# Kernel optimization log

Measured on AMD Instinct MI355X. Metric: run time of the kernel, lower is better.

## Reference

```python
import jax, jax.numpy as jnp
import numpy as np

N, E, G, D = 100000, 1600000, 1000, 32
EPS = 1e-5


def setup_inputs() -> dict:
    key = jax.random.key(0)
    ks = jax.random.split(key, 24)
    inp = {
        'h': jax.random.normal(ks[0], (N, D), dtype=jnp.float32),
        'src': jax.random.randint(ks[1], (E,), 0, N, dtype=jnp.int32),
        'dst': jax.random.randint(ks[2], (E,), 0, N, dtype=jnp.int32),
        'graph_id': jnp.sort(jax.random.randint(ks[3], (N,), 0, G, dtype=jnp.int32)),
    }
    dims = [D, 32, 32, 32, 1]
    ki = 4
    for i in range(4):
        inp[f'conv_w{i}'] = jax.random.normal(ks[ki], (dims[i], dims[i + 1]), dtype=jnp.float32) * 0.1; ki += 1
        inp[f'conv_b{i}'] = jax.random.normal(ks[ki], (dims[i + 1],), dtype=jnp.float32) * 0.1; ki += 1
        inp[f'bn_g{i}'] = jnp.ones((dims[i + 1],), dtype=jnp.float32)
        inp[f'bn_b{i}'] = jnp.zeros((dims[i + 1],), dtype=jnp.float32)
    mlp_dims = [D + 32 + 32 + 32 + 1, 128, 64, 1]  # 129 -> 128 -> 64 -> 1
    for i in range(3):
        inp[f'mlp_w{i}'] = jax.random.normal(ks[ki], (mlp_dims[i], mlp_dims[i + 1]), dtype=jnp.float32) * 0.1; ki += 1
        inp[f'mlp_b{i}'] = jax.random.normal(ks[ki], (mlp_dims[i + 1],), dtype=jnp.float32) * 0.1; ki += 1
    return inp


def _mean_agg(x, src, dst):
    # DGL update_all(copy_u, mean): h'_v = mean of h_u over in-neighbors u of v
    deg = jax.ops.segment_sum(jnp.ones((src.shape[0],), x.dtype), dst, num_segments=N)
    agg = jax.ops.segment_sum(x[src], dst, num_segments=N)
    return agg / jnp.maximum(deg, 1.0)[:, None]


def _bn(x, g, b):
    # BatchNorm1d in training mode: batch statistics over node dim
    m = x.mean(axis=0)
    v = x.var(axis=0)
    return g * (x - m) * jax.lax.rsqrt(v + EPS) + b


def reference(h, src, dst, graph_id,
              conv_w0, conv_b0, conv_w1, conv_b1, conv_w2, conv_b2, conv_w3, conv_b3,
              bn_g0, bn_b0, bn_g1, bn_b1, bn_g2, bn_b2, bn_g3, bn_b3,
              mlp_w0, mlp_b0, mlp_w1, mlp_b1, mlp_w2, mlp_b2):
    conv = [(conv_w0, conv_b0), (conv_w1, conv_b1), (conv_w2, conv_b2), (conv_w3, conv_b3)]
    bn = [(bn_g0, bn_b0), (bn_g1, bn_b1), (bn_g2, bn_b2), (bn_g3, bn_b3)]
    h_list = [h]
    x = h
    for (w, b), (g, bb) in zip(conv, bn):
        x = _mean_agg(x, src, dst) @ w + b      # GCNConv
        x = jax.nn.relu(_bn(x, g, bb))           # BN + ReLU
        h_list.append(x)
    h_final = jnp.concatenate(h_list, axis=1)    # [N, 129]
    # dgl.mean_nodes: per-graph mean pool
    cnt = jax.ops.segment_sum(jnp.ones((N,), h_final.dtype), graph_id, num_segments=G)
    hg = jax.ops.segment_sum(h_final, graph_id, num_segments=G) / jnp.maximum(cnt, 1.0)[:, None]
    hg = jax.nn.relu(hg @ mlp_w0 + mlp_b0)
    hg = jax.nn.relu(hg @ mlp_w1 + mlp_b1)
    hg = hg @ mlp_w2 + mlp_b2
    return hg.reshape(-1)                         # [G]
```

## Files before the change

### kernel.cpp

```cpp
#include <hip/hip_runtime.h>

#define NSLOT 32
#define BN_EPS 1e-5f
#define NSB 256
#define BKBITS 8
#define BKN 256
#define MAXBUCK 512

static inline int cdiv_h(int a, int b) { return (a + b - 1) / b; }

__device__ __forceinline__ float4 f4add(float4 a, float4 b) {
    return make_float4(a.x + b.x, a.y + b.y, a.z + b.z, a.w + b.w);
}

__device__ __forceinline__ unsigned bf16rtn(float x) {
    unsigned u = __float_as_uint(x);
    return (u + 0x7FFFu + ((u >> 16) & 1u)) >> 16;
}
__device__ __forceinline__ unsigned bf16pack2(float lo, float hi) {
    return bf16rtn(lo) | (bf16rtn(hi) << 16);
}

__device__ __forceinline__ int blk_excl_scan256(int v, int t) {
    __shared__ int wsum[4];
    int l = t & 63, w = t >> 6;
    int incl = v;
#pragma unroll
    for (int off = 1; off < 64; off <<= 1) {
        int o = __shfl_up(incl, off, 64);
        if (l >= off) incl += o;
    }
    if (l == 63) wsum[w] = incl;
    __syncthreads();
    int wofs = 0;
#pragma unroll
    for (int i = 0; i < 4; i++) wofs += (i < w) ? wsum[i] : 0;
    __syncthreads();
    return wofs + incl - v;
}

__device__ __forceinline__ int blk_excl_scan512(int v, int t) {
    __shared__ int wsum8[8];
    int l = t & 63, w = t >> 6;
    int incl = v;
#pragma unroll
    for (int off = 1; off < 64; off <<= 1) {
        int o = __shfl_up(incl, off, 64);
        if (l >= off) incl += o;
    }
    if (l == 63) wsum8[w] = incl;
    __syncthreads();
    int wofs = 0;
#pragma unroll
    for (int i = 0; i < 8; i++) wofs += (i < w) ? wsum8[i] : 0;
    __syncthreads();
    return wofs + incl - v;
}


__global__ __launch_bounds__(256) void k_hist(const int* __restrict__ dst, int* __restrict__ histT,
                                              int E, int nbuck, int chunk) {
    __shared__ int bins[MAXBUCK];
    int k = blockIdx.x, t = threadIdx.x;
    for (int b = t; b < nbuck; b += 256) bins[b] = 0;
    __syncthreads();
    int lo = k * chunk, hi = lo + chunk; if (hi > E) hi = E;
    for (int i = lo + t; i < hi; i += 256) atomicAdd(&bins[dst[i] >> BKBITS], 1);
    __syncthreads();
    for (int b = t; b < nbuck; b += 256) histT[k * nbuck + b] = bins[b];
}


__global__ __launch_bounds__(256) void k_scanA(const int* __restrict__ histT, int* __restrict__ prefixB,
                                               int* __restrict__ totalP, int* __restrict__ totalU, int nbuck) {
    int b = blockIdx.x, k = threadIdx.x;
    int c = histT[k * nbuck + b];
    int pad = (c + 15) & ~15;
    int ep = blk_excl_scan256(pad, k);
    prefixB[b * NSB + k] = ep;
    int ec = blk_excl_scan256(c, k);
    if (k == NSB - 1) { totalP[b] = ep + pad; totalU[b] = ec + c; }
}

__global__ __launch_bounds__(512) void k_scanB(const int* __restrict__ totalP, const int* __restrict__ totalU,
                                               int* __restrict__ baseP, int* __restrict__ baseU, int nbuck) {
    int t = threadIdx.x;
    int vp = (t < nbuck) ? totalP[t] : 0;
    int vu = (t < nbuck) ? totalU[t] : 0;
    int ep = blk_excl_scan512(vp, t);
    int eu = blk_excl_scan512(vu, t);
    if (t < nbuck) { baseP[t] = ep; baseU[t] = eu; }
}


__global__ __launch_bounds__(256) void k_scatter2(const int* __restrict__ src, const int* __restrict__ dst,
                                                  const int* __restrict__ baseP, const int* __restrict__ prefixB,
                                                  unsigned* __restrict__ ebuf, int E, int nbuck, int chunk) {
    __shared__ int cur[MAXBUCK];
    int k = blockIdx.x, t = threadIdx.x;
    for (int b = t; b < nbuck; b += 256) cur[b] = baseP[b] + prefixB[b * NSB + k];
    __syncthreads();
    int lo = k * chunk, hi = lo + chunk; if (hi > E) hi = E;
    for (int i = lo + t; i < hi; i += 256) {
        int d = dst[i], s = src[i];
        int b = d >> BKBITS;
        int pos = atomicAdd(&cur[b], 1);
        ebuf[pos] = ((unsigned)(d & (BKN - 1)) << 24) | (unsigned)s;
    }
}


__global__ __launch_bounds__(256) void k_sortb(const unsigned* __restrict__ ebuf, const int* __restrict__ histT,
                                               const int* __restrict__ baseP, const int* __restrict__ prefixB,
                                               const int* __restrict__ baseU,
                                               int* __restrict__ col, int* __restrict__ rs, int* __restrict__ re,
                                               int nbuck, int N) {
    __shared__ int binCnt[BKN], binStart[BKN], cursor[BKN];
    __shared__ int cellBase[NSB], cellCnt[NSB];
    int b = blockIdx.x, t = threadIdx.x;
    cellBase[t] = baseP[b] + prefixB[b * NSB + t];
    cellCnt[t]  = histT[t * nbuck + b];
    binCnt[t] = 0; cursor[t] = 0;
    __syncthreads();
    {
        int cb = cellBase[t], cc = cellCnt[t];
        for (int j = 0; j < cc; j++) atomicAdd(&binCnt[ebuf[cb + j] >> 24], 1);
    }
    __syncthreads();
    int bs = blk_excl_scan256(binCnt[t], t);
    binStart[t] = bs;
    __syncthreads();
    int colBase = baseU[b];
    {
        int cb = cellBase[t], cc = cellCnt[t];
        for (int j = 0; j < cc; j++) {
            unsigned e = ebuf[cb + j];
            int l = e >> 24;
            int pos = binStart[l] + atomicAdd(&cursor[l], 1);
            col[colBase + pos] = (int)(e & 0xFFFFFFu);
        }
    }
    int node = b * BKN + t;
    if (node < N) {
        rs[node] = colBase + binStart[t];
        re[node] = colBase + binStart[t] + binCnt[t];
    }
}


__global__ __launch_bounds__(256) void k_gstart(const int* __restrict__ gid, int* __restrict__ gstart, int n, int G) {
    int i = blockIdx.x * 256 + threadIdx.x;
    if (i >= n) return;
    int g = gid[i];
    int gp = (i == 0) ? -1 : gid[i - 1];
    for (int x = gp + 1; x <= g; ++x) gstart[x] = i;
    if (i == n - 1) { for (int x = g + 1; x <= G; ++x) gstart[x] = n; }
}


template <int AFF>
__global__ __launch_bounds__(256) void k_transform(const float* __restrict__ xin, const float* __restrict__ W,
                                                   const float* __restrict__ cA, const float* __restrict__ cC,
                                                   uint4* __restrict__ pb, int n) {
    __shared__ float sW[32][32];
    __shared__ float sA[32], sC[32];
    int t = threadIdx.x;
    for (int i = t; i < 1024; i += 256) sW[i >> 5][i & 31] = W[i];
    if (AFF && t < 32) { sA[t] = cA[t]; sC[t] = cC[t]; }
    __syncthreads();
    int node = blockIdx.x * 256 + t;
    if (node >= n) return;
    float x[32];
    const float4* s4 = (const float4*)(xin + (size_t)node * 32);
#pragma unroll
    for (int q = 0; q < 8; q++) {
        float4 v = s4[q];
        x[4*q] = v.x; x[4*q+1] = v.y; x[4*q+2] = v.z; x[4*q+3] = v.w;
    }
    if (AFF) {
#pragma unroll
        for (int k = 0; k < 32; k++) {
            float v = sA[k] * x[k] + sC[k];
            x[k] = v > 0.f ? v : 0.f;
        }
    }
    float acc[32];
#pragma unroll
    for (int f = 0; f < 32; f++) acc[f] = 0.f;
#pragma unroll
    for (int k = 0; k < 32; k++) {
        float xv = x[k];
#pragma unroll
        for (int f = 0; f < 32; f++) acc[f] += xv * sW[k][f];
    }
    uint4* d4 = pb + (size_t)node * 4;
#pragma unroll
    for (int q = 0; q < 4; q++) {
        uint4 o;
        o.x = bf16pack2(acc[8*q+0], acc[8*q+1]);
        o.y = bf16pack2(acc[8*q+2], acc[8*q+3]);
        o.z = bf16pack2(acc[8*q+4], acc[8*q+5]);
        o.w = bf16pack2(acc[8*q+6], acc[8*q+7]);
        d4[q] = o;
    }
}

__global__ __launch_bounds__(256) void k_transform3(const float* __restrict__ y2, const float* __restrict__ w3,
                                                    const float* __restrict__ cA, const float* __restrict__ cC,
                                                    float* __restrict__ p3, int n) {
    __shared__ float sw[32], sA[32], sC[32];
    int t = threadIdx.x;
    if (t < 32) { sw[t] = w3[t]; sA[t] = cA[t]; sC[t] = cC[t]; }
    __syncthreads();
    int i = blockIdx.x * 256 + t;
    if (i >= n) return;
    const float4* x4 = (const float4*)(y2 + (size_t)i * 32);
    float acc = 0.f;
#pragma unroll
    for (int q = 0; q < 8; q++) {
        float4 v = x4[q];
        float vv[4] = {v.x, v.y, v.z, v.w};
#pragma unroll
        for (int r = 0; r < 4; r++) {
            int k = q * 4 + r;
            float xv = sA[k] * vv[r] + sC[k];
            xv = xv > 0.f ? xv : 0.f;
            acc += xv * sw[k];
        }
    }
    p3[i] = acc;
}


__global__ __launch_bounds__(256) void k_aggregate(const uint4* __restrict__ pb, const int* __restrict__ rs,
                                                   const int* __restrict__ re, const int* __restrict__ col,
                                                   const float* __restrict__ bias,
                                                   float4* __restrict__ y4, float* __restrict__ sSum,
                                                   float* __restrict__ sSq, int n) {
    int t = threadIdx.x;
    int lane = t & 3;
    int grp = t >> 2;
    int node = blockIdx.x * 64 + grp;
    float accA[8], accB[8];
#pragma unroll
    for (int q = 0; q < 8; q++) { accA[q] = 0.f; accB[q] = 0.f; }
    float vout[8];
#pragma unroll
    for (int q = 0; q < 8; q++) vout[q] = 0.f;
    if (node < n) {
        int s0 = rs[node], s1 = re[node];
        int j = s0;
#define GATH(vv, c) uint4 vv = pb[(size_t)(c) * 4 + lane]
#define ACC(dst, vv) \
        dst[0] += __uint_as_float((vv).x << 16); dst[1] += __uint_as_float((vv).x & 0xFFFF0000u); \
        dst[2] += __uint_as_float((vv).y << 16); dst[3] += __uint_as_float((vv).y & 0xFFFF0000u); \
        dst[4] += __uint_as_float((vv).z << 16); dst[5] += __uint_as_float((vv).z & 0xFFFF0000u); \
        dst[6] += __uint_as_float((vv).w << 16); dst[7] += __uint_as_float((vv).w & 0xFFFF0000u)
        for (; j + 8 <= s1; j += 8) {
            int c0 = col[j], c1 = col[j + 1], c2 = col[j + 2], c3 = col[j + 3];
            int c4 = col[j + 4], c5 = col[j + 5], c6 = col[j + 6], c7 = col[j + 7];
            GATH(g0, c0); GATH(g1, c1); GATH(g2, c2); GATH(g3, c3);
            GATH(g4, c4); GATH(g5, c5); GATH(g6, c6); GATH(g7, c7);
            ACC(accA, g0); ACC(accB, g1); ACC(accA, g2); ACC(accB, g3);
            ACC(accA, g4); ACC(accB, g5); ACC(accA, g6); ACC(accB, g7);
        }
        for (; j < s1; ++j) {
            GATH(g, col[j]);
            ACC(accA, g);
        }
#undef GATH
#undef ACC
        int deg = s1 - s0;
        float inv = (deg > 0) ? 1.f / (float)deg : 1.f;
        const float4* b4 = (const float4*)bias;
        float4 b0 = b4[lane * 2], b1 = b4[lane * 2 + 1];
        vout[0] = (accA[0] + accB[0]) * inv + b0.x;
        vout[1] = (accA[1] + accB[1]) * inv + b0.y;
        vout[2] = (accA[2] + accB[2]) * inv + b0.z;
        vout[3] = (accA[3] + accB[3]) * inv + b0.w;
        vout[4] = (accA[4] + accB[4]) * inv + b1.x;
        vout[5] = (accA[5] + accB[5]) * inv + b1.y;
        vout[6] = (accA[6] + accB[6]) * inv + b1.z;
        vout[7] = (accA[7] + accB[7]) * inv + b1.w;
        y4[(size_t)node * 8 + lane * 2]     = make_float4(vout[0], vout[1], vout[2], vout[3]);
        y4[(size_t)node * 8 + lane * 2 + 1] = make_float4(vout[4], vout[5], vout[6], vout[7]);
    }
    __shared__ float sS[64][32];
    __shared__ float sQ[64][32];
    ((float4*)&sS[grp][lane * 8])[0] = make_float4(vout[0], vout[1], vout[2], vout[3]);
    ((float4*)&sS[grp][lane * 8])[1] = make_float4(vout[4], vout[5], vout[6], vout[7]);
    ((float4*)&sQ[grp][lane * 8])[0] = make_float4(vout[0]*vout[0], vout[1]*vout[1], vout[2]*vout[2], vout[3]*vout[3]);
    ((float4*)&sQ[grp][lane * 8])[1] = make_float4(vout[4]*vout[4], vout[5]*vout[5], vout[6]*vout[6], vout[7]*vout[7]);
    __syncthreads();
    if (t < 32) {
        float S = 0.f, Q = 0.f;
#pragma unroll
        for (int g2 = 0; g2 < 64; g2++) { S += sS[g2][t]; Q += sQ[g2][t]; }
        int slot = blockIdx.x & (NSLOT - 1);
        atomicAdd(&sSum[slot * 32 + t], S);
        atomicAdd(&sSq[slot * 32 + t], Q);
    }
}

__global__ __launch_bounds__(256) void k_aggregate3(const float* __restrict__ p3, const int* __restrict__ rs,
                                                    const int* __restrict__ re, const int* __restrict__ col,
                                                    const float* __restrict__ b1,
                                                    float* __restrict__ y3, float* __restrict__ sSum,
                                                    float* __restrict__ sSq, int n) {
    int i = blockIdx.x * 256 + threadIdx.x;
    float lsum = 0.f, lsq = 0.f;
    if (i < n) {
        int s0 = rs[i], s1 = re[i];
        float a0 = 0.f, a1 = 0.f, a2 = 0.f, a3 = 0.f;
        int j = s0;
        for (; j + 4 <= s1; j += 4) {
            int c0 = col[j], c1 = col[j + 1], c2 = col[j + 2], c3 = col[j + 3];
            a0 += p3[c0]; a1 += p3[c1]; a2 += p3[c2]; a3 += p3[c3];
        }
        for (; j < s1; ++j) a0 += p3[col[j]];
        float acc = (a0 + a1) + (a2 + a3);
        float inv = (s1 > s0) ? 1.f / (float)(s1 - s0) : 1.f;
        float v = acc * inv + b1[0];
        y3[i] = v; lsum = v; lsq = v * v;
    }
    __shared__ float sS[256], sQ[256];
    int t = threadIdx.x;
    sS[t] = lsum; sQ[t] = lsq;
    __syncthreads();
    for (int s = 128; s > 0; s >>= 1) {
        if (t < s) { sS[t] += sS[t + s]; sQ[t] += sQ[t + s]; }
        __syncthreads();
    }
    if (t == 0) {
        int slot = blockIdx.x & (NSLOT - 1);
        atomicAdd(&sSum[slot * 32], sS[0]);
        atomicAdd(&sSq[slot * 32], sQ[0]);
    }
}


__global__ void k_stats(const float* __restrict__ sSum, const float* __restrict__ sSq,
                        const float* __restrict__ g, const float* __restrict__ b,
                        float* __restrict__ cA, float* __restrict__ cC, int C, float invN) {
    int f = threadIdx.x;
    if (f < C) {
        float S = 0.f, Q = 0.f;
        for (int s = 0; s < NSLOT; s++) { S += sSum[s * 32 + f]; Q += sSq[s * 32 + f]; }
        float m = S * invN;
        float var = Q * invN - m * m;
        if (var < 0.f) var = 0.f;
        float inv = rsqrtf(var + BN_EPS);
        float a = g[f] * inv;
        cA[f] = a;
        cC[f] = b[f] - m * a;
    }
}


__global__ __launch_bounds__(256) void k_pool_mlp(const float* __restrict__ h, const float* __restrict__ y0,
                                                  const float* __restrict__ y1, const float* __restrict__ y2,
                                                  const float* __restrict__ y3, const float* __restrict__ cA,
                                                  const float* __restrict__ cC, const int* __restrict__ gstart,
                                                  const float* __restrict__ w0, const float* __restrict__ b0,
                                                  const float* __restrict__ w1, const float* __restrict__ b1,
                                                  const float* __restrict__ w2, const float* __restrict__ b2,
                                                  float* __restrict__ out) {
    int g = blockIdx.x;
    int t = threadIdx.x;
    int s0 = gstart[g], s1 = gstart[g + 1];
    int lane = t & 31, slot = t >> 5;
    int arr = lane >> 3, sub = lane & 7;
    const float* bases0 = (arr == 0) ? h : (arr == 1) ? y0 : (arr == 2) ? y1 : y2;
    const float4* bp = (const float4*)bases0;
    float4 a4 = make_float4(1.f, 1.f, 1.f, 1.f);
    float4 c4 = make_float4(0.f, 0.f, 0.f, 0.f);
    bool aff = (arr > 0);
    if (aff) {
        a4 = ((const float4*)cA)[(arr - 1) * 8 + sub];
        c4 = ((const float4*)cC)[(arr - 1) * 8 + sub];
    }
    float4 acc = make_float4(0.f, 0.f, 0.f, 0.f);
    for (int n = s0 + slot; n < s1; n += 8) {
        float4 v = bp[(size_t)n * 8 + sub];
        if (aff) {
            float vx = fmaf(a4.x, v.x, c4.x); vx = vx > 0.f ? vx : 0.f;
            float vy = fmaf(a4.y, v.y, c4.y); vy = vy > 0.f ? vy : 0.f;
            float vz = fmaf(a4.z, v.z, c4.z); vz = vz > 0.f ? vz : 0.f;
            float vw = fmaf(a4.w, v.w, c4.w); vw = vw > 0.f ? vw : 0.f;
            v = make_float4(vx, vy, vz, vw);
        }
        acc = f4add(acc, v);
    }
    __shared__ float sP[8][128];
    __shared__ float sY[8];
    ((float4*)&sP[slot][lane * 4])[0] = acc;
    if (t < 8) {
        float a = cA[96], c = cC[96], s = 0.f;
        for (int n = s0 + t; n < s1; n += 8) {
            float v = fmaf(a, y3[n], c);
            s += v > 0.f ? v : 0.f;
        }
        sY[t] = s;
    }
    __syncthreads();
    __shared__ float hg[129];
    __shared__ float hid1[128];
    __shared__ float hid2[64];
    float inv = (s1 > s0) ? 1.f / (float)(s1 - s0) : 1.f;
    if (t < 128) {
        float S = 0.f;
#pragma unroll
        for (int s = 0; s < 8; s++) S += sP[s][t];
        hg[t] = S * inv;
    } else if (t == 128) {
        float S = 0.f;
#pragma unroll
        for (int s = 0; s < 8; s++) S += sY[s];
        hg[128] = S * inv;
    }
    __syncthreads();
    if (t < 128) {
        float a = b0[t];
        for (int i = 0; i < 129; i++) a += hg[i] * w0[i * 128 + t];
        hid1[t] = a > 0.f ? a : 0.f;
    }
    __syncthreads();
    if (t < 64) {
        float a = b1[t];
        for (int i = 0; i < 128; i++) a += hid1[i] * w1[i * 64 + t];
        hid2[t] = a > 0.f ? a : 0.f;
    }
    __syncthreads();
    if (t < 64) {
        float v = hid2[t] * w2[t];
        for (int off = 32; off > 0; off >>= 1) v += __shfl_down(v, off, 64);
        if (t == 0) out[g] = v + b2[0];
    }
}


extern "C" void kernel_launch(void* const* d_in, const int* in_sizes, int n_in,
                              void* d_out, int out_size, void* d_ws, size_t ws_size,
                              hipStream_t stream) {
    const float* h   = (const float*)d_in[0];
    const int* src   = (const int*)d_in[1];
    const int* dst   = (const int*)d_in[2];
    const int* gid   = (const int*)d_in[3];
    const float* convw[4], *convb[4], *bng[4], *bnb[4];
    for (int i = 0; i < 4; i++) {
        convw[i] = (const float*)d_in[4 + 4 * i];
        convb[i] = (const float*)d_in[5 + 4 * i];
        bng[i]   = (const float*)d_in[6 + 4 * i];
        bnb[i]   = (const float*)d_in[7 + 4 * i];
    }
    const float* mw0 = (const float*)d_in[20];
    const float* mb0 = (const float*)d_in[21];
    const float* mw1 = (const float*)d_in[22];
    const float* mb1 = (const float*)d_in[23];
    const float* mw2 = (const float*)d_in[24];
    const float* mb2 = (const float*)d_in[25];

    const int N = in_sizes[0] / 32;
    const int E = in_sizes[1];
    const int G = out_size;
    const int nbuck = cdiv_h(N, BKN);
    const int chunk = cdiv_h(E, NSB);

    char* ws = (char*)d_ws;
    size_t off = 0;
    auto alloc = [&](size_t bytes) -> void* {
        void* p = ws + off;
        off += (bytes + 511) & ~(size_t)511;
        return p;
    };
    int* histT   = (int*)alloc((size_t)NSB * nbuck * 4);
    int* prefixB = (int*)alloc((size_t)nbuck * NSB * 4);
    int* totalP  = (int*)alloc((size_t)nbuck * 4);
    int* totalU  = (int*)alloc((size_t)nbuck * 4);
    int* basePp  = (int*)alloc((size_t)nbuck * 4);
    int* baseUp  = (int*)alloc((size_t)nbuck * 4);
    size_t ebufE = (size_t)E + (size_t)16 * NSB * nbuck;
    size_t ovl   = ebufE * 4;
    size_t pB    = (size_t)N * 64;
    if (pB > ovl) ovl = pB;
    unsigned* ebuf = (unsigned*)alloc(ovl);
    uint4* pb    = (uint4*)ebuf;
    int* col     = (int*)alloc((size_t)E * 4);
    int* rs      = (int*)alloc((size_t)N * 4);
    int* re      = (int*)alloc((size_t)N * 4);
    int* gstart  = (int*)alloc((size_t)(G + 1) * 4);
    float* y0    = (float*)alloc((size_t)N * 32 * 4);
    float* y1    = (float*)alloc((size_t)N * 32 * 4);
    float* y2    = (float*)alloc((size_t)N * 32 * 4);
    float* y3    = (float*)alloc((size_t)N * 4);
    float* sSum  = (float*)alloc((size_t)4 * NSLOT * 32 * 4);
    float* sSq   = (float*)alloc((size_t)4 * NSLOT * 32 * 4);
    float* cAa   = (float*)alloc((size_t)4 * 32 * 4);
    float* cCc   = (float*)alloc((size_t)4 * 32 * 4);
    (void)ws_size; (void)n_in;

    const int NB_N = cdiv_h(N, 256);
    const int NB_AG = cdiv_h(N, 64);
    const float invN = 1.f / (float)N;

    hipMemsetAsync(sSum, 0, (size_t)4 * NSLOT * 32 * 4, stream);
    hipMemsetAsync(sSq, 0, (size_t)4 * NSLOT * 32 * 4, stream);

    k_hist<<<NSB, 256, 0, stream>>>(dst, histT, E, nbuck, chunk);
    k_scanA<<<nbuck, 256, 0, stream>>>(histT, prefixB, totalP, totalU, nbuck);
    k_scanB<<<1, 512, 0, stream>>>(totalP, totalU, basePp, baseUp, nbuck);
    k_scatter2<<<NSB, 256, 0, stream>>>(src, dst, basePp, prefixB, ebuf, E, nbuck, chunk);
    k_sortb<<<nbuck, 256, 0, stream>>>(ebuf, histT, basePp, prefixB, baseUp, col, rs, re, nbuck, N);
    k_gstart<<<NB_N, 256, 0, stream>>>(gid, gstart, N, G);

    k_transform<0><<<NB_N, 256, 0, stream>>>(h, convw[0], nullptr, nullptr, pb, N);
    k_aggregate<<<NB_AG, 256, 0, stream>>>(pb, rs, re, col, convb[0], (float4*)y0,
                                           sSum + 0 * NSLOT * 32, sSq + 0 * NSLOT * 32, N);
    k_stats<<<1, 32, 0, stream>>>(sSum + 0 * NSLOT * 32, sSq + 0 * NSLOT * 32, bng[0], bnb[0], cAa + 0, cCc + 0, 32, invN);
    k_transform<1><<<NB_N, 256, 0, stream>>>(y0, convw[1], cAa + 0, cCc + 0, pb, N);
    k_aggregate<<<NB_AG, 256, 0, stream>>>(pb, rs, re, col, convb[1], (float4*)y1,
                                           sSum + 1 * NSLOT * 32, sSq + 1 * NSLOT * 32, N);
    k_stats<<<1, 32, 0, stream>>>(sSum + 1 * NSLOT * 32, sSq + 1 * NSLOT * 32, bng[1], bnb[1], cAa + 32, cCc + 32, 32, invN);
    k_transform<1><<<NB_N, 256, 0, stream>>>(y1, convw[2], cAa + 32, cCc + 32, pb, N);
    k_aggregate<<<NB_AG, 256, 0, stream>>>(pb, rs, re, col, convb[2], (float4*)y2,
                                           sSum + 2 * NSLOT * 32, sSq + 2 * NSLOT * 32, N);
    k_stats<<<1, 32, 0, stream>>>(sSum + 2 * NSLOT * 32, sSq + 2 * NSLOT * 32, bng[2], bnb[2], cAa + 64, cCc + 64, 32, invN);
    k_transform3<<<NB_N, 256, 0, stream>>>(y2, convw[3], cAa + 64, cCc + 64, (float*)pb, N);
    k_aggregate3<<<NB_N, 256, 0, stream>>>((float*)pb, rs, re, col, convb[3], y3,
                                           sSum + 3 * NSLOT * 32, sSq + 3 * NSLOT * 32, N);
    k_stats<<<1, 32, 0, stream>>>(sSum + 3 * NSLOT * 32, sSq + 3 * NSLOT * 32, bng[3], bnb[3], cAa + 96, cCc + 96, 1, invN);

    k_pool_mlp<<<G, 256, 0, stream>>>(h, y0, y1, y2, y3, cAa, cCc, gstart,
                                      mw0, mb0, mw1, mb1, mw2, mb2, (float*)d_out);
}
```

Before: 339.3 us.

## Fold BN stats, memset and gstart into neighbours; stage col indices in LDS

Removes the four single-block BN-statistics kernels by recomputing the BN scale/shift per block inside the consuming transform and pool kernels. It also folds the stats-buffer memsets into k_hist and the graph-start computation into k_scanA, which cuts about seven launches and their serialization gaps. Separately, k_aggregate now cooperatively loads each block's contiguous CSR column range into shared memory before gathering, replacing scattered global index reads. The cost is redundant coefficient recomputation in every block, extra LDS use that may lower occupancy, and removal of the 8-wide unrolled path when the range exceeds 2048 edges.

```diff
diff --git a/kernel.cpp b/kernel.cpp
--- a/kernel.cpp
+++ b/kernel.cpp
@@ -57,11 +57,30 @@
     return wofs + incl - v;
 }
 
+__device__ __forceinline__ void bn_coef(const float* __restrict__ sSum, const float* __restrict__ sSq,
+                                        const float* __restrict__ bg, const float* __restrict__ bb,
+                                        float invN, int ch, float* aOut, float* cOut) {
+    float S = 0.f, Q = 0.f;
+#pragma unroll
+    for (int s = 0; s < NSLOT; s++) { S += sSum[s * 32 + ch]; Q += sSq[s * 32 + ch]; }
+    float m = S * invN;
+    float var = Q * invN - m * m;
+    if (var < 0.f) var = 0.f;
+    float iv = rsqrtf(var + BN_EPS);
+    float a = bg[ch] * iv;
+    *aOut = a;
+    *cOut = bb[ch] - m * a;
+}
+
 
 __global__ __launch_bounds__(256) void k_hist(const int* __restrict__ dst, int* __restrict__ histT,
+                                              float* __restrict__ sSum, float* __restrict__ sSq,
                                               int E, int nbuck, int chunk) {
     __shared__ int bins[MAXBUCK];
     int k = blockIdx.x, t = threadIdx.x;
+    if (k == 0) {
+        for (int i = t; i < 4 * NSLOT * 32; i += 256) { sSum[i] = 0.f; sSq[i] = 0.f; }
+    }
     for (int b = t; b < nbuck; b += 256) bins[b] = 0;
     __syncthreads();
     int lo = k * chunk, hi = lo + chunk; if (hi > E) hi = E;
@@ -72,8 +91,17 @@
 
 
 __global__ __launch_bounds__(256) void k_scanA(const int* __restrict__ histT, int* __restrict__ prefixB,
-                                               int* __restrict__ totalP, int* __restrict__ totalU, int nbuck) {
+                                               int* __restrict__ totalP, int* __restrict__ totalU,
+                                               const int* __restrict__ gid, int* __restrict__ gstart,
+                                               int nbuck, int N, int G) {
     int b = blockIdx.x, k = threadIdx.x;
+    int i = b * 256 + k;
+    if (i < N) {
+        int g = gid[i];
+        int gp = (i == 0) ? -1 : gid[i - 1];
+        for (int x = gp + 1; x <= g; ++x) gstart[x] = i;
+        if (i == N - 1) { for (int x = g + 1; x <= G; ++x) gstart[x] = N; }
+    }
     int c = histT[k * nbuck + b];
     int pad = (c + 15) & ~15;
     int ep = blk_excl_scan256(pad, k);
@@ -148,25 +176,16 @@
 }
 
 
-__global__ __launch_bounds__(256) void k_gstart(const int* __restrict__ gid, int* __restrict__ gstart, int n, int G) {
-    int i = blockIdx.x * 256 + threadIdx.x;
-    if (i >= n) return;
-    int g = gid[i];
-    int gp = (i == 0) ? -1 : gid[i - 1];
-    for (int x = gp + 1; x <= g; ++x) gstart[x] = i;
-    if (i == n - 1) { for (int x = g + 1; x <= G; ++x) gstart[x] = n; }
-}
-
-
 template <int AFF>
 __global__ __launch_bounds__(256) void k_transform(const float* __restrict__ xin, const float* __restrict__ W,
-                                                   const float* __restrict__ cA, const float* __restrict__ cC,
-                                                   uint4* __restrict__ pb, int n) {
+                                                   const float* __restrict__ sSum, const float* __restrict__ sSq,
+                                                   const float* __restrict__ bg, const float* __restrict__ bb,
+                                                   uint4* __restrict__ pb, int n, float invN) {
     __shared__ float sW[32][32];
     __shared__ float sA[32], sC[32];
     int t = threadIdx.x;
     for (int i = t; i < 1024; i += 256) sW[i >> 5][i & 31] = W[i];
-    if (AFF && t < 32) { sA[t] = cA[t]; sC[t] = cC[t]; }
+    if (AFF && t < 32) bn_coef(sSum, sSq, bg, bb, invN, t, &sA[t], &sC[t]);
     __syncthreads();
     int node = blockIdx.x * 256 + t;
     if (node >= n) return;
@@ -206,11 +225,12 @@
 }
 
 __global__ __launch_bounds__(256) void k_transform3(const float* __restrict__ y2, const float* __restrict__ w3,
-                                                    const float* __restrict__ cA, const float* __restrict__ cC,
-                                                    float* __restrict__ p3, int n) {
+                                                    const float* __restrict__ sSum, const float* __restrict__ sSq,
+                                                    const float* __restrict__ bg, const float* __restrict__ bb,
+                                                    float* __restrict__ p3, int n, float invN) {
     __shared__ float sw[32], sA[32], sC[32];
     int t = threadIdx.x;
-    if (t < 32) { sw[t] = w3[t]; sA[t] = cA[t]; sC[t] = cC[t]; }
+    if (t < 32) { sw[t] = w3[t]; bn_coef(sSum, sSq, bg, bb, invN, t, &sA[t], &sC[t]); }
     __syncthreads();
     int i = blockIdx.x * 256 + t;
     if (i >= n) return;
@@ -237,10 +257,22 @@
                                                    const float* __restrict__ bias,
                                                    float4* __restrict__ y4, float* __restrict__ sSum,
                                                    float* __restrict__ sSq, int n) {
+    __shared__ int scol[2048];
     int t = threadIdx.x;
     int lane = t & 3;
     int grp = t >> 2;
-    int node = blockIdx.x * 64 + grp;
+    int node0 = blockIdx.x * 64;
+    int node = node0 + grp;
+    int base0 = 0, len = 0;
+    if (node0 < n) {
+        int last = node0 + 63; if (last > n - 1) last = n - 1;
+        base0 = rs[node0];
+        len = re[last] - base0;
+    }
+    bool lds = (len > 0 && len <= 2048);
+    if (lds) { for (int i = t; i < len; i += 256) scol[i] = col[base0 + i]; }
+    __syncthreads();
+
     float accA[8], accB[8];
 #pragma unroll
     for (int q = 0; q < 8; q++) { accA[q] = 0.f; accB[q] = 0.f; }
@@ -249,24 +281,25 @@
     for (int q = 0; q < 8; q++) vout[q] = 0.f;
     if (node < n) {
         int s0 = rs[node], s1 = re[node];
-        int j = s0;
 #define GATH(vv, c) uint4 vv = pb[(size_t)(c) * 4 + lane]
 #define ACC(dst, vv) \
         dst[0] += __uint_as_float((vv).x << 16); dst[1] += __uint_as_float((vv).x & 0xFFFF0000u); \
         dst[2] += __uint_as_float((vv).y << 16); dst[3] += __uint_as_float((vv).y & 0xFFFF0000u); \
         dst[4] += __uint_as_float((vv).z << 16); dst[5] += __uint_as_float((vv).z & 0xFFFF0000u); \
         dst[6] += __uint_as_float((vv).w << 16); dst[7] += __uint_as_float((vv).w & 0xFFFF0000u)
-        for (; j + 8 <= s1; j += 8) {
-            int c0 = col[j], c1 = col[j + 1], c2 = col[j + 2], c3 = col[j + 3];
-            int c4 = col[j + 4], c5 = col[j + 5], c6 = col[j + 6], c7 = col[j + 7];
-            GATH(g0, c0); GATH(g1, c1); GATH(g2, c2); GATH(g3, c3);
-            GATH(g4, c4); GATH(g5, c5); GATH(g6, c6); GATH(g7, c7);
-            ACC(accA, g0); ACC(accB, g1); ACC(accA, g2); ACC(accB, g3);
-            ACC(accA, g4); ACC(accB, g5); ACC(accA, g6); ACC(accB, g7);
-        }
-        for (; j < s1; ++j) {
-            GATH(g, col[j]);
-            ACC(accA, g);
+        if (lds) {
+            int j = s0 - base0, j1 = s1 - base0;
+            for (; j + 8 <= j1; j += 8) {
+                int c0 = scol[j], c1 = scol[j + 1], c2 = scol[j + 2], c3 = scol[j + 3];
+                int c4 = scol[j + 4], c5 = scol[j + 5], c6 = scol[j + 6], c7 = scol[j + 7];
+                GATH(g0, c0); GATH(g1, c1); GATH(g2, c2); GATH(g3, c3);
+                GATH(g4, c4); GATH(g5, c5); GATH(g6, c6); GATH(g7, c7);
+                ACC(accA, g0); ACC(accB, g1); ACC(accA, g2); ACC(accB, g3);
+                ACC(accA, g4); ACC(accB, g5); ACC(accA, g6); ACC(accB, g7);
+            }
+            for (; j < j1; ++j) { GATH(g, scol[j]); ACC(accA, g); }
+        } else {
+            for (int j = s0; j < s1; ++j) { GATH(g, col[j]); ACC(accA, g); }
         }
 #undef GATH
 #undef ACC
@@ -339,34 +372,30 @@
 }
 
 
-__global__ void k_stats(const float* __restrict__ sSum, const float* __restrict__ sSq,
-                        const float* __restrict__ g, const float* __restrict__ b,
-                        float* __restrict__ cA, float* __restrict__ cC, int C, float invN) {
-    int f = threadIdx.x;
-    if (f < C) {
-        float S = 0.f, Q = 0.f;
-        for (int s = 0; s < NSLOT; s++) { S += sSum[s * 32 + f]; Q += sSq[s * 32 + f]; }
-        float m = S * invN;
-        float var = Q * invN - m * m;
-        if (var < 0.f) var = 0.f;
-        float inv = rsqrtf(var + BN_EPS);
-        float a = g[f] * inv;
-        cA[f] = a;
-        cC[f] = b[f] - m * a;
-    }
-}
-
-
 __global__ __launch_bounds__(256) void k_pool_mlp(const float* __restrict__ h, const float* __restrict__ y0,
                                                   const float* __restrict__ y1, const float* __restrict__ y2,
-                                                  const float* __restrict__ y3, const float* __restrict__ cA,
-                                                  const float* __restrict__ cC, const int* __restrict__ gstart,
+                                                  const float* __restrict__ y3,
+                                                  const float* __restrict__ sSum, const float* __restrict__ sSq,
+                                                  const float* __restrict__ bg0, const float* __restrict__ bb0,
+                                                  const float* __restrict__ bg1, const float* __restrict__ bb1,
+                                                  const float* __restrict__ bg2, const float* __restrict__ bb2,
+                                                  const float* __restrict__ bg3, const float* __restrict__ bb3,
+                                                  const int* __restrict__ gstart,
                                                   const float* __restrict__ w0, const float* __restrict__ b0,
                                                   const float* __restrict__ w1, const float* __restrict__ b1,
                                                   const float* __restrict__ w2, const float* __restrict__ b2,
-                                                  float* __restrict__ out) {
+                                                  float* __restrict__ out, float invN) {
+    __shared__ float pcA[128], pcC[128];
     int g = blockIdx.x;
     int t = threadIdx.x;
+    if (t < 97) {
+        int layer = (t == 96) ? 3 : (t >> 5);
+        int ch = t & 31;
+        const float* bg = (layer == 0) ? bg0 : (layer == 1) ? bg1 : (layer == 2) ? bg2 : bg3;
+        const float* bb = (layer == 0) ? bb0 : (layer == 1) ? bb1 : (layer == 2) ? bb2 : bb3;
+        bn_coef(sSum + layer * NSLOT * 32, sSq + layer * NSLOT * 32, bg, bb, invN, ch, &pcA[t], &pcC[t]);
+    }
+    __syncthreads();
     int s0 = gstart[g], s1 = gstart[g + 1];
     int lane = t & 31, slot = t >> 5;
     int arr = lane >> 3, sub = lane & 7;
@@ -376,8 +405,8 @@
     float4 c4 = make_float4(0.f, 0.f, 0.f, 0.f);
     bool aff = (arr > 0);
     if (aff) {
-        a4 = ((const float4*)cA)[(arr - 1) * 8 + sub];
-        c4 = ((const float4*)cC)[(arr - 1) * 8 + sub];
+        a4 = ((const float4*)pcA)[(arr - 1) * 8 + sub];
+        c4 = ((const float4*)pcC)[(arr - 1) * 8 + sub];
     }
     float4 acc = make_float4(0.f, 0.f, 0.f, 0.f);
     for (int n = s0 + slot; n < s1; n += 8) {
@@ -395,7 +424,7 @@
     __shared__ float sY[8];
     ((float4*)&sP[slot][lane * 4])[0] = acc;
     if (t < 8) {
-        float a = cA[96], c = cC[96], s = 0.f;
+        float a = pcA[96], c = pcC[96], s = 0.f;
         for (int n = s0 + t; n < s1; n += 8) {
             float v = fmaf(a, y3[n], c);
             s += v > 0.f ? v : 0.f;
@@ -495,41 +524,35 @@
     float* y3    = (float*)alloc((size_t)N * 4);
     float* sSum  = (float*)alloc((size_t)4 * NSLOT * 32 * 4);
     float* sSq   = (float*)alloc((size_t)4 * NSLOT * 32 * 4);
-    float* cAa   = (float*)alloc((size_t)4 * 32 * 4);
-    float* cCc   = (float*)alloc((size_t)4 * 32 * 4);
     (void)ws_size; (void)n_in;
 
     const int NB_N = cdiv_h(N, 256);
     const int NB_AG = cdiv_h(N, 64);
     const float invN = 1.f / (float)N;
 
-    hipMemsetAsync(sSum, 0, (size_t)4 * NSLOT * 32 * 4, stream);
-    hipMemsetAsync(sSq, 0, (size_t)4 * NSLOT * 32 * 4, stream);
-
-    k_hist<<<NSB, 256, 0, stream>>>(dst, histT, E, nbuck, chunk);
-    k_scanA<<<nbuck, 256, 0, stream>>>(histT, prefixB, totalP, totalU, nbuck);
+    k_hist<<<NSB, 256, 0, stream>>>(dst, histT, sSum, sSq, E, nbuck, chunk);
+    k_scanA<<<nbuck, 256, 0, stream>>>(histT, prefixB, totalP, totalU, gid, gstart, nbuck, N, G);
     k_scanB<<<1, 512, 0, stream>>>(totalP, totalU, basePp, baseUp, nbuck);
     k_scatter2<<<NSB, 256, 0, stream>>>(src, dst, basePp, prefixB, ebuf, E, nbuck, chunk);
     k_sortb<<<nbuck, 256, 0, stream>>>(ebuf, histT, basePp, prefixB, baseUp, col, rs, re, nbuck, N);
-    k_gstart<<<NB_N, 256, 0, stream>>>(gid, gstart, N, G);
-
-    k_transform<0><<<NB_N, 256, 0, stream>>>(h, convw[0], nullptr, nullptr, pb, N);
+
+    k_transform<0><<<NB_N, 256, 0, stream>>>(h, convw[0], nullptr, nullptr, nullptr, nullptr, pb, N, invN);
     k_aggregate<<<NB_AG, 256, 0, stream>>>(pb, rs, re, col, convb[0], (float4*)y0,
                                            sSum + 0 * NSLOT * 32, sSq + 0 * NSLOT * 32, N);
-    k_stats<<<1, 32, 0, stream>>>(sSum + 0 * NSLOT * 32, sSq + 0 * NSLOT * 32, bng[0], bnb[0], cAa + 0, cCc + 0, 32, invN);
-    k_transform<1><<<NB_N, 256, 0, stream>>>(y0, convw[1], cAa + 0, cCc + 0, pb, N);
+    k_transform<1><<<NB_N, 256, 0, stream>>>(y0, convw[1], sSum + 0 * NSLOT * 32, sSq + 0 * NSLOT * 32,
+                                             bng[0], bnb[0], pb, N, invN);
     k_aggregate<<<NB_AG, 256, 0, stream>>>(pb, rs, re, col, convb[1], (float4*)y1,
                                            sSum + 1 * NSLOT * 32, sSq + 1 * NSLOT * 32, N);
-    k_stats<<<1, 32, 0, stream>>>(sSum + 1 * NSLOT * 32, sSq + 1 * NSLOT * 32, bng[1], bnb[1], cAa + 32, cCc + 32, 32, invN);
-    k_transform<1><<<NB_N, 256, 0, stream>>>(y1, convw[2], cAa + 32, cCc + 32, pb, N);
+    k_transform<1><<<NB_N, 256, 0, stream>>>(y1, convw[2], sSum + 1 * NSLOT * 32, sSq + 1 * NSLOT * 32,
+                                             bng[1], bnb[1], pb, N, invN);
     k_aggregate<<<NB_AG, 256, 0, stream>>>(pb, rs, re, col, convb[2], (float4*)y2,
                                            sSum + 2 * NSLOT * 32, sSq + 2 * NSLOT * 32, N);
-    k_stats<<<1, 32, 0, stream>>>(sSum + 2 * NSLOT * 32, sSq + 2 * NSLOT * 32, bng[2], bnb[2], cAa + 64, cCc + 64, 32, invN);
-    k_transform3<<<NB_N, 256, 0, stream>>>(y2, convw[3], cAa + 64, cCc + 64, (float*)pb, N);
+    k_transform3<<<NB_N, 256, 0, stream>>>(y2, convw[3], sSum + 2 * NSLOT * 32, sSq + 2 * NSLOT * 32,
+                                           bng[2], bnb[2], (float*)pb, N, invN);
     k_aggregate3<<<NB_N, 256, 0, stream>>>((float*)pb, rs, re, col, convb[3], y3,
                                            sSum + 3 * NSLOT * 32, sSq + 3 * NSLOT * 32, N);
-    k_stats<<<1, 32, 0, stream>>>(sSum + 3 * NSLOT * 32, sSq + 3 * NSLOT * 32, bng[3], bnb[3], cAa + 96, cCc + 96, 1, invN);
-
-    k_pool_mlp<<<G, 256, 0, stream>>>(h, y0, y1, y2, y3, cAa, cCc, gstart,
-                                      mw0, mb0, mw1, mb1, mw2, mb2, (float*)d_out);
-}
+
+    k_pool_mlp<<<G, 256, 0, stream>>>(h, y0, y1, y2, y3, sSum, sSq,
+                                      bng[0], bnb[0], bng[1], bnb[1], bng[2], bnb[2], bng[3], bnb[3],
+                                      gstart, mw0, mb0, mw1, mb1, mw2, mb2, (float*)d_out, invN);
+}
```

Measured after the change: 319.8 us. 1.06x faster.
